# Kernel optimization log

Hardware: AMD Instinct MI355X
Metric: run time of the kernel (lower is better)

## Reference

```python
import jax, jax.numpy as jnp
import numpy as np

B, T, D = 8, 1024, 1024

def setup_inputs() -> dict:
    key = jax.random.key(0)
    ks = jax.random.split(key, 9)
    s = D ** -0.5
    return {
        "x": jax.random.normal(ks[0], (B, T, D), dtype=jnp.float32),
        "w_q": jax.random.normal(ks[1], (D, D), dtype=jnp.float32) * s,
        "b_q": jax.random.normal(ks[2], (D,), dtype=jnp.float32) * 0.02,
        "w_k": jax.random.normal(ks[3], (D, D), dtype=jnp.float32) * s,
        "b_k": jax.random.normal(ks[4], (D,), dtype=jnp.float32) * 0.02,
        "w_v": jax.random.normal(ks[5], (D, D), dtype=jnp.float32) * s,
        "b_v": jax.random.normal(ks[6], (D,), dtype=jnp.float32) * 0.02,
        "w_o": jax.random.normal(ks[7], (D, D), dtype=jnp.float32) * s,
        "b_o": jax.random.normal(ks[8], (D,), dtype=jnp.float32) * 0.02,
    }

def reference(x, w_q, b_q, w_k, b_k, w_v, b_v, w_o, b_o):
    d = x.shape[-1]
    scale = jnp.asarray(d, x.dtype) ** -0.5
    q = jnp.einsum('btd,ed->bte', x, w_q) + b_q  # nn.Linear: x @ W^T + b
    k = jnp.einsum('btd,ed->bte', x, w_k) + b_k
    v = jnp.einsum('btd,ed->bte', x, w_v) + b_v
    t = x.shape[1]
    causal = jnp.tril(jnp.ones((t, t), dtype=bool))  # (T, T)
    scores = jnp.einsum('bqd,bkd->bqk', q, k) * scale
    scores = jnp.where(causal, scores, -jnp.inf)
    attn = jax.nn.softmax(scores, axis=-1)  # max-subtraction folded in
    out = jnp.einsum('bqk,bkd->bqd', attn, v)
    return jnp.einsum('btd,ed->bte', out, w_o) + b_o
```

## Files before the change

kernel.cpp:

```cpp
#include <hip/hip_runtime.h>

typedef unsigned short u16;
typedef __attribute__((ext_vector_type(8))) short short8;
typedef __attribute__((ext_vector_type(4))) float f32x4;


__device__ __forceinline__ u16 f2bf(float f) {
  unsigned u = __builtin_bit_cast(unsigned, f);
  u += 0x7fffu + ((u >> 16) & 1u);
  return (u16)(u >> 16);
}

__device__ __forceinline__ void gload16(const void* g, void* l) {
  __builtin_amdgcn_global_load_lds(
      (const __attribute__((address_space(1))) unsigned*)g,
      (__attribute__((address_space(3))) unsigned*)l, 16, 0, 0);
}


#define PTILE(RB_C, RB_N, DOSTAGE, VM, LAST)                                  \
  {                                                                           \
    char* cA = sA0 + cur * 49152;                                             \
                                                       \
    if (DOSTAGE) {                                                            \
      const int ns = (cur + 2 >= 3) ? cur - 1 : cur + 2;                      \
      char* dA = sA0 + ns * 49152;                                            \
      _Pragma("unroll") for (int j = 0; j < 3; ++j) {                         \
        gload16(ga[j], dA + la[j]); ga[j] += 64; }                            \
    }                                                                         \
    _Pragma("unroll") for (int kk = 0; kk < 2; ++kk)                          \
      _Pragma("unroll") for (int i = 0; i < 2; ++i) {                         \
        const int rm = wr + 32 + i * 16 + l16;                                \
        a1f[kk][i] = *(const short8*)(cA + rm * 128 +                         \
            (((kk << 2) + quad) ^ (rm & 7)) * 16);                            \
      }                                                                       \
    asm volatile("s_waitcnt lgkmcnt(4)" ::: "memory");                        \
    __builtin_amdgcn_sched_barrier(0);                                        \
    __builtin_amdgcn_s_setprio(1);                                            \
    _Pragma("unroll") for (int kk = 0; kk < 2; ++kk)                          \
      _Pragma("unroll") for (int i = 0; i < 2; ++i)                           \
        _Pragma("unroll") for (int j = 0; j < 4; ++j)                         \
          acc[i][j] = __builtin_amdgcn_mfma_f32_16x16x32_bf16(                \
              a0f[kk][i], RB_C[kk][j], acc[i][j], 0, 0, 0);                   \
    __builtin_amdgcn_s_setprio(0);                                            \
                                                       \
    if (DOSTAGE) {                                                            \
      const int ns = (cur + 2 >= 3) ? cur - 1 : cur + 2;                      \
      char* dA = sA0 + ns * 49152; char* dB = dA + 32768;                     \
      gload16(ga[3], dA + la[3]); ga[3] += 64;                                \
      _Pragma("unroll") for (int j = 0; j < 2; ++j) {                         \
        gload16(gb[j], dB + lb[j]); gb[j] += 64; }                            \
    }                                                                         \
    if (!(LAST)) {                                                            \
      asm volatile("s_waitcnt vmcnt(" #VM ") lgkmcnt(0)" ::: "memory");       \
      __builtin_amdgcn_s_barrier();                                           \
      asm volatile("" ::: "memory");                                          \
      const int nc = (cur + 1 >= 3) ? 0 : cur + 1;                            \
      char* nA = sA0 + nc * 49152; char* nB = nA + 32768;                     \
      _Pragma("unroll") for (int kk = 0; kk < 2; ++kk)                        \
        _Pragma("unroll") for (int j = 0; j < 4; ++j) {                       \
          const int rn = wc + j * 16 + l16;                                   \
          RB_N[kk][j] = *(const short8*)(nB + rn * 128 +                      \
              (((kk << 2) + quad) ^ (rn & 7)) * 16);                          \
        }                                                                     \
      _Pragma("unroll") for (int kk = 0; kk < 2; ++kk)                        \
        _Pragma("unroll") for (int i = 0; i < 2; ++i) {                       \
          const int rm = wr + i * 16 + l16;                                   \
          a0f[kk][i] = *(const short8*)(nA + rm * 128 +                       \
              (((kk << 2) + quad) ^ (rm & 7)) * 16);                          \
        }                                                                     \
    } else {                                                                  \
      asm volatile("s_waitcnt lgkmcnt(0)" ::: "memory");                      \
    }                                                                         \
    __builtin_amdgcn_sched_barrier(0);                                        \
    __builtin_amdgcn_s_setprio(1);                                            \
    _Pragma("unroll") for (int kk = 0; kk < 2; ++kk)                          \
      _Pragma("unroll") for (int i = 0; i < 2; ++i)                           \
        _Pragma("unroll") for (int j = 0; j < 4; ++j)                         \
          acc[2 + i][j] = __builtin_amdgcn_mfma_f32_16x16x32_bf16(            \
              a1f[kk][i], RB_C[kk][j], acc[2 + i][j], 0, 0, 0);               \
    __builtin_amdgcn_s_setprio(0);                                            \
    cur = (cur + 1 >= 3) ? 0 : cur + 1;                                       \
  }

__device__ __forceinline__ void gemm_256x128(
    const u16* __restrict__ A, const u16* __restrict__ B,
    int m0, int n0, int ntiles, char* smem, f32x4 acc[4][4])
{
  const int tid  = threadIdx.x;
  const int lane = tid & 63;
  const int quad = lane >> 4;
  const int l16  = lane & 15;
  const int wave = tid >> 6;
  const int wr   = (wave >> 1) << 6;
  const int wc   = (wave & 1) << 6;

  const u16* ga[4]; int la[4];
  const u16* gb[2]; int lb[2];
#pragma unroll
  for (int j = 0; j < 4; ++j) {
    const int L = j * 512 + tid;
    const int r = L >> 3;
    const int c = (L & 7) ^ (r & 7);
    la[j] = L * 16;
    ga[j] = A + (size_t)(m0 + r) * 1024 + c * 8;
  }
#pragma unroll
  for (int j = 0; j < 2; ++j) {
    const int L = j * 512 + tid;
    const int r = L >> 3;
    const int c = (L & 7) ^ (r & 7);
    lb[j] = L * 16;
    gb[j] = B + (size_t)(n0 + r) * 1024 + c * 8;
  }
  char* const sA0 = smem;

  short8 bfr0[2][4], bfr1[2][4];
  short8 a0f[2][2], a1f[2][2];

  {
    char* dA = sA0; char* dB = sA0 + 32768;
#pragma unroll
    for (int j = 0; j < 4; ++j) { gload16(ga[j], dA + la[j]); ga[j] += 64; }
#pragma unroll
    for (int j = 0; j < 2; ++j) { gload16(gb[j], dB + lb[j]); gb[j] += 64; }
    dA = sA0 + 49152; dB = dA + 32768;
#pragma unroll
    for (int j = 0; j < 4; ++j) { gload16(ga[j], dA + la[j]); ga[j] += 64; }
#pragma unroll
    for (int j = 0; j < 2; ++j) { gload16(gb[j], dB + lb[j]); gb[j] += 64; }
  }
  asm volatile("s_waitcnt vmcnt(6)" ::: "memory");
  __builtin_amdgcn_s_barrier();
  asm volatile("" ::: "memory");
  {
    char* nA = sA0; char* nB = sA0 + 32768;
#pragma unroll
    for (int kk = 0; kk < 2; ++kk)
#pragma unroll
      for (int j = 0; j < 4; ++j) {
        const int rn = wc + j * 16 + l16;
        bfr0[kk][j] = *(const short8*)(nB + rn * 128 + (((kk << 2) + quad) ^ (rn & 7)) * 16);
      }
#pragma unroll
    for (int kk = 0; kk < 2; ++kk)
#pragma unroll
      for (int i = 0; i < 2; ++i) {
        const int rm = wr + i * 16 + l16;
        a0f[kk][i] = *(const short8*)(nA + rm * 128 + (((kk << 2) + quad) ^ (rm & 7)) * 16);
      }
  }

  int cur = 0;
  const int npair = (ntiles >> 1) - 1;
#pragma unroll 1
  for (int it = 0; it < npair; ++it) {
    PTILE(bfr0, bfr1, true, 6, false);
    PTILE(bfr1, bfr0, true, 6, false);
  }
  PTILE(bfr0, bfr1, false, 0, false);
  PTILE(bfr1, bfr0, false, 0, true);
  __syncthreads();
}

#define ACC_ZERO4(acc) { _Pragma("unroll") for (int i=0;i<4;++i) \
  _Pragma("unroll") for (int j=0;j<4;++j) \
  _Pragma("unroll") for (int r=0;r<4;++r) acc[i][j][r]=0.f; }

__device__ __forceinline__ void store256x128_bf16(
    f32x4 acc[4][4], const float* bias, int n0,
    u16* C, int m0, char* smem)
{
  const int tid = threadIdx.x, lane = tid & 63, wave = tid >> 6;
  const int quad = lane >> 4, l16 = lane & 15;
  const int wr = (wave >> 1) << 6, wc = (wave & 1) << 6;
  u16* t = (u16*)smem;
#pragma unroll
  for (int j = 0; j < 4; ++j) {
    const int nn = wc + j * 16 + l16;
    const float bj = bias[n0 + nn];
#pragma unroll
    for (int i = 0; i < 4; ++i) {
      const int mm = wr + i * 16 + quad * 4;
#pragma unroll
      for (int r = 0; r < 4; ++r)
        t[(mm + r) * 136 + nn] = f2bf(acc[i][j][r] + bj);
    }
  }
  __syncthreads();
#pragma unroll
  for (int it = 0; it < 8; ++it) {
    const int L = it * 512 + tid;
    const int mm = L >> 4, cc = L & 15;
    *(uint4*)(C + (size_t)(m0 + mm) * 1024 + n0 + cc * 8) =
        *(const uint4*)(t + mm * 136 + cc * 8);
  }
}

__global__ __launch_bounds__(256) void cast_inputs(
    const float* __restrict__ x,  const float* __restrict__ wq,
    const float* __restrict__ wk, const float* __restrict__ wv,
    const float* __restrict__ wo,
    u16* xb, u16* wqb, u16* wkb, u16* wvb, u16* wob, float* rsum)
{
  int b = blockIdx.x;
  if (b < 8) {
    float4 z = {0.f, 0.f, 0.f, 0.f};
    *(float4*)(rsum + (b * 256 + threadIdx.x) * 4) = z;
  }
  const float* src; u16* dst; int base;
  if (b < 4096) { src = x; dst = xb; base = b * 2048; }
  else {
    int r = (b - 4096) >> 9, bb = (b - 4096) & 511;
    base = bb * 2048;
    src = (r == 0) ? wq : (r == 1) ? wk : (r == 2) ? wv : wo;
    dst = (r == 0) ? wqb : (r == 1) ? wkb : (r == 2) ? wvb : wob;
  }
  int i0 = base + threadIdx.x * 8;
  float4 f0 = *(const float4*)(src + i0);
  float4 f1 = *(const float4*)(src + i0 + 4);
  short8 o;
  o[0]=(short)f2bf(f0.x); o[1]=(short)f2bf(f0.y); o[2]=(short)f2bf(f0.z); o[3]=(short)f2bf(f0.w);
  o[4]=(short)f2bf(f1.x); o[5]=(short)f2bf(f1.y); o[6]=(short)f2bf(f1.z); o[7]=(short)f2bf(f1.w);
  *(short8*)(dst + i0) = o;
}

__global__ __launch_bounds__(512, 2) void proj_qkv(
    const u16* __restrict__ xb,
    const u16* __restrict__ wqb, const u16* __restrict__ wkb, const u16* __restrict__ wvb,
    const float* __restrict__ bq, const float* __restrict__ bk, const float* __restrict__ bv,
    u16* q, u16* k, u16* vt)
{
  __shared__ char smem[147456];
  const int z = blockIdx.y;
  const u16* W = (z == 0) ? wqb : (z == 1) ? wkb : wvb;
  const float* bias = (z == 0) ? bq : (z == 1) ? bk : bv;
  const int id = blockIdx.x;
  const int m0 = ((id & 7) * 4 + ((id >> 3) & 3)) * 256;
  const int n0 = (id >> 5) * 128;

  f32x4 acc[4][4]; ACC_ZERO4(acc);
  gemm_256x128(xb, W, m0, n0, 16, smem, acc);

  if (z < 2) {
    store256x128_bf16(acc, bias, n0, (z == 0) ? q : k, m0, smem);
  } else {
    const int tid = threadIdx.x, lane = tid & 63, wave = tid >> 6;
    const int quad = lane >> 4, l16 = lane & 15;
    const int wr = (wave >> 1) << 6, wc = (wave & 1) << 6;
    u16* t = (u16*)smem;
#pragma unroll
    for (int j = 0; j < 4; ++j) {
      const int nn = wc + j * 16 + l16;
      const float bj = bias[n0 + nn];
#pragma unroll
      for (int i = 0; i < 4; ++i) {
        const int mm = wr + i * 16 + quad * 4;
#pragma unroll
        for (int r = 0; r < 4; ++r)
          t[nn * 264 + mm + r] = f2bf(acc[i][j][r] + bj);
      }
    }
    __syncthreads();
    const int b = m0 >> 10, t0 = m0 & 1023;
#pragma unroll
    for (int it = 0; it < 8; ++it) {
      const int L = it * 512 + tid;
      const int nn = L >> 5, cc = L & 31;
      *(uint4*)(vt + ((size_t)b << 20) + (size_t)(n0 + nn) * 1024 + t0 + cc * 8) =
          *(const uint4*)(t + nn * 264 + cc * 8);
    }
  }
}

__global__ __launch_bounds__(512, 2) void qk_exp256(
    const u16* __restrict__ q, const u16* __restrict__ k,
    u16* __restrict__ probs, float* __restrict__ rowsum)
{
  __shared__ char smem[147456];
  const int id = blockIdx.x;
  const int b = id / 20;
  const int t = id - b * 20;
  const int qi = (t < 2) ? 0 : (t < 6) ? 1 : (t < 12) ? 2 : 3;
  const int pre = (qi == 0) ? 0 : (qi == 1) ? 2 : (qi == 2) ? 6 : 12;
  const int kt = t - pre;
  const int m0 = qi * 256, n0 = kt * 128;
  const u16* A = q + ((size_t)b << 20);
  const u16* B = k + ((size_t)b << 20);

  f32x4 acc[4][4]; ACC_ZERO4(acc);
  gemm_256x128(A, B, m0, n0, 16, smem, acc);

  const int tid = threadIdx.x, lane = tid & 63, wave = tid >> 6;
  const int quad = lane >> 4, l16 = lane & 15;
  const int wr = (wave >> 1) << 6, wc = (wave & 1) << 6;

  float part[4][4];
#pragma unroll
  for (int i = 0; i < 4; ++i)
#pragma unroll
    for (int r = 0; r < 4; ++r) part[i][r] = 0.f;

  u16* tl = (u16*)smem;
#pragma unroll
  for (int j = 0; j < 4; ++j) {
    const int nn = wc + j * 16 + l16;
#pragma unroll
    for (int i = 0; i < 4; ++i) {
      const int mm = wr + i * 16 + quad * 4;
#pragma unroll
      for (int r = 0; r < 4; ++r) {
        float e = __expf(acc[i][j][r] * 0.03125f);
        if ((n0 + nn) > (m0 + mm + r)) e = 0.f;
        part[i][r] += e;
        tl[(mm + r) * 136 + nn] = f2bf(e);
      }
    }
  }
  float* rs = rowsum + b * 1024 + m0;
#pragma unroll
  for (int i = 0; i < 4; ++i)
#pragma unroll
    for (int r = 0; r < 4; ++r) {
      float v = part[i][r];
      v += __shfl_xor(v, 1); v += __shfl_xor(v, 2);
      v += __shfl_xor(v, 4); v += __shfl_xor(v, 8);
      if (l16 == 0) atomicAdd(rs + wr + i * 16 + quad * 4 + r, v);
    }
  __syncthreads();
  u16* C = probs + ((size_t)b << 20);
#pragma unroll
  for (int it = 0; it < 8; ++it) {
    const int L = it * 512 + tid;
    const int mm = L >> 4, cc = L & 15;
    *(uint4*)(C + (size_t)(m0 + mm) * 1024 + n0 + cc * 8) =
        *(const uint4*)(tl + mm * 136 + cc * 8);
  }
}

__global__ __launch_bounds__(512, 2) void pv256(
    const u16* __restrict__ probs, const u16* __restrict__ vt,
    const float* __restrict__ rowsum, u16* __restrict__ o)
{
  __shared__ char smem[147456];
  const int id = blockIdx.x;
  const int b = id & 7;
  const int u = id >> 3;
  const int qi = 3 - (u & 3);
  const int nb = u >> 2;
  const int m0 = qi * 256, n0 = nb * 128;
  const int nt = (qi + 1) * 4;
  const u16* A = probs + ((size_t)b << 20);
  const u16* B = vt + ((size_t)b << 20);

  f32x4 acc[4][4]; ACC_ZERO4(acc);
  gemm_256x128(A, B, m0, n0, nt, smem, acc);

  const int tid = threadIdx.x, lane = tid & 63, wave = tid >> 6;
  const int quad = lane >> 4, l16 = lane & 15;
  const int wr = (wave >> 1) << 6, wc = (wave & 1) << 6;
  const float* rs = rowsum + b * 1024 + m0;
  u16* tl = (u16*)smem;
#pragma unroll
  for (int i = 0; i < 4; ++i)
#pragma unroll
    for (int r = 0; r < 4; ++r) {
      const int mm = wr + i * 16 + quad * 4 + r;
      const float inv = 1.0f / rs[mm];
#pragma unroll
      for (int j = 0; j < 4; ++j)
        tl[mm * 136 + wc + j * 16 + l16] = f2bf(acc[i][j][r] * inv);
    }
  __syncthreads();
  u16* C = o + ((size_t)b << 20);
#pragma unroll
  for (int it = 0; it < 8; ++it) {
    const int L = it * 512 + tid;
    const int mm = L >> 4, cc = L & 15;
    *(uint4*)(C + (size_t)(m0 + mm) * 1024 + n0 + cc * 8) =
        *(const uint4*)(tl + mm * 136 + cc * 8);
  }
}

__global__ __launch_bounds__(512, 2) void proj_o(
    const u16* __restrict__ ob, const u16* __restrict__ wob,
    const float* __restrict__ bo, float* __restrict__ out)
{
  __shared__ char smem[147456];
  const int id = blockIdx.x;
  const int m0 = ((id & 7) * 4 + ((id >> 3) & 3)) * 256;
  const int n0 = (id >> 5) * 128;
  f32x4 acc[4][4]; ACC_ZERO4(acc);
  gemm_256x128(ob, wob, m0, n0, 16, smem, acc);

  const int tid = threadIdx.x, lane = tid & 63, wave = tid >> 6;
  const int quad = lane >> 4, l16 = lane & 15;
  const int wr = (wave >> 1) << 6, wc = (wave & 1) << 6;
  float* tf = (float*)smem;
#pragma unroll
  for (int j = 0; j < 4; ++j) {
    const int nn = wc + j * 16 + l16;
    const float bj = bo[n0 + nn];
#pragma unroll
    for (int i = 0; i < 4; ++i)
#pragma unroll
      for (int r = 0; r < 4; ++r)
        tf[(wr + i * 16 + quad * 4 + r) * 132 + nn] = acc[i][j][r] + bj;
  }
  __syncthreads();
#pragma unroll
  for (int it = 0; it < 16; ++it) {
    const int L = it * 512 + tid;
    const int mm = L >> 5, cc = L & 31;
    *(float4*)(out + (size_t)(m0 + mm) * 1024 + n0 + cc * 4) =
        *(const float4*)(tf + mm * 132 + cc * 4);
  }
}

extern "C" void kernel_launch(void* const* d_in, const int* in_sizes, int n_in,
                              void* d_out, int out_size, void* d_ws, size_t ws_size,
                              hipStream_t stream) {
  const float* x  = (const float*)d_in[0];
  const float* wq = (const float*)d_in[1];
  const float* bq = (const float*)d_in[2];
  const float* wk = (const float*)d_in[3];
  const float* bk = (const float*)d_in[4];
  const float* wv = (const float*)d_in[5];
  const float* bv = (const float*)d_in[6];
  const float* wo = (const float*)d_in[7];
  const float* bo = (const float*)d_in[8];
  float* out = (float*)d_out;

  char* ws = (char*)d_ws;
  const size_t MB = 1u << 20;
  u16*  xb  = (u16*)(ws);
  u16*  wqb = (u16*)(ws + 16*MB);
  u16*  wkb = (u16*)(ws + 18*MB);
  u16*  wvb = (u16*)(ws + 20*MB);
  u16*  wob = (u16*)(ws + 22*MB);
  u16*  qb  = (u16*)(ws + 24*MB);
  u16*  kb  = (u16*)(ws + 40*MB);
  u16*  vtb = (u16*)(ws + 56*MB);
  u16*  pr  = (u16*)(ws + 72*MB);
  float* rsum = (float*)(ws + 88*MB);

  cast_inputs<<<6144, 256, 0, stream>>>(x, wq, wk, wv, wo, xb, wqb, wkb, wvb, wob, rsum);
  proj_qkv<<<dim3(256, 3), 512, 0, stream>>>(xb, wqb, wkb, wvb, bq, bk, bv, qb, kb, vtb);
  qk_exp256<<<160, 512, 0, stream>>>(qb, kb, pr, rsum);
  pv256<<<256, 512, 0, stream>>>(pr, vtb, rsum, xb );
  proj_o<<<256, 512, 0, stream>>>(xb, wob, bo, out);
}
```

Measured before the change: 211.9 us.

## Enlarge QKV projection GEMM tile to 256x256 with double-buffered LDS pipeline

Adds a new 256x256-tile GEMM routine for the QKV projection. It uses a two-buffer LDS pipeline and each wave computes a 128x64 sub-tile, which halves the grid to 128x3 blocks. The larger tile raises operand reuse and cuts how often the activations are re-read from global memory. In exchange each thread holds twice the accumulator registers, and with 384 blocks the work may fill the device's compute units less evenly. The Q/K and V-transpose epilogues are rewritten for the wider tile.

```diff
diff --git a/kernel.cpp b/kernel.cpp
--- a/kernel.cpp
+++ b/kernel.cpp
@@ -16,6 +16,8 @@
       (const __attribute__((address_space(1))) unsigned*)g,
       (__attribute__((address_space(3))) unsigned*)l, 16, 0, 0);
 }
+
+#define MFMA16(a, b, c) __builtin_amdgcn_mfma_f32_16x16x32_bf16(a, b, c, 0, 0, 0)
 
 
 #define PTILE(RB_C, RB_N, DOSTAGE, VM, LAST)                                  \
@@ -40,8 +42,7 @@
     _Pragma("unroll") for (int kk = 0; kk < 2; ++kk)                          \
       _Pragma("unroll") for (int i = 0; i < 2; ++i)                           \
         _Pragma("unroll") for (int j = 0; j < 4; ++j)                         \
-          acc[i][j] = __builtin_amdgcn_mfma_f32_16x16x32_bf16(                \
-              a0f[kk][i], RB_C[kk][j], acc[i][j], 0, 0, 0);                   \
+          acc[i][j] = MFMA16(a0f[kk][i], RB_C[kk][j], acc[i][j]);             \
     __builtin_amdgcn_s_setprio(0);                                            \
                                                        \
     if (DOSTAGE) {                                                            \
@@ -77,8 +78,7 @@
     _Pragma("unroll") for (int kk = 0; kk < 2; ++kk)                          \
       _Pragma("unroll") for (int i = 0; i < 2; ++i)                           \
         _Pragma("unroll") for (int j = 0; j < 4; ++j)                         \
-          acc[2 + i][j] = __builtin_amdgcn_mfma_f32_16x16x32_bf16(            \
-              a1f[kk][i], RB_C[kk][j], acc[2 + i][j], 0, 0, 0);               \
+          acc[2 + i][j] = MFMA16(a1f[kk][i], RB_C[kk][j], acc[2 + i][j]);     \
     __builtin_amdgcn_s_setprio(0);                                            \
     cur = (cur + 1 >= 3) ? 0 : cur + 1;                                       \
   }
@@ -163,7 +163,156 @@
   __syncthreads();
 }
 
+
+#define T256(CB, NB, BC, BN, DOSTAGE, LAST)                                   \
+  {                                                                           \
+         \
+    if (DOSTAGE) {                                                            \
+      _Pragma("unroll") for (int j = 0; j < 4; ++j)                           \
+        gload16(gA + j * 65536, (NB) + j * 8192 + t16);                       \
+    }                                                                         \
+    _Pragma("unroll") for (int kk = 0; kk < 2; ++kk)                          \
+      _Pragma("unroll") for (int i = 0; i < 2; ++i) {                         \
+        const int rm = wr + (2 + i) * 16 + l16;                               \
+        aod[kk][i] = *(const short8*)((CB) + rm * 128 +                       \
+            (((kk << 2) + quad) ^ (rm & 7)) * 16);                            \
+      }                                                                       \
+    asm volatile("s_waitcnt lgkmcnt(4)" ::: "memory");                        \
+    __builtin_amdgcn_sched_barrier(0);                                        \
+    __builtin_amdgcn_s_setprio(1);                                            \
+    _Pragma("unroll") for (int kk = 0; kk < 2; ++kk)                          \
+      _Pragma("unroll") for (int i = 0; i < 2; ++i)                           \
+        _Pragma("unroll") for (int j = 0; j < 4; ++j)                         \
+          acc[i][j] = MFMA16(aev[kk][i], BC[kk][j], acc[i][j]);               \
+    __builtin_amdgcn_s_setprio(0);                                            \
+         \
+    if (DOSTAGE) {                                                            \
+      _Pragma("unroll") for (int j = 0; j < 4; ++j)                           \
+        gload16(gB + j * 65536, (NB) + 32768 + j * 8192 + t16);               \
+      gA += 64; gB += 64;                                                     \
+    }                                                                         \
+    _Pragma("unroll") for (int kk = 0; kk < 2; ++kk)                          \
+      _Pragma("unroll") for (int i = 0; i < 2; ++i) {                         \
+        const int rm = wr + (4 + i) * 16 + l16;                               \
+        aev[kk][i] = *(const short8*)((CB) + rm * 128 +                       \
+            (((kk << 2) + quad) ^ (rm & 7)) * 16);                            \
+      }                                                                       \
+    asm volatile("s_waitcnt lgkmcnt(4)" ::: "memory");                        \
+    __builtin_amdgcn_sched_barrier(0);                                        \
+    __builtin_amdgcn_s_setprio(1);                                            \
+    _Pragma("unroll") for (int kk = 0; kk < 2; ++kk)                          \
+      _Pragma("unroll") for (int i = 0; i < 2; ++i)                           \
+        _Pragma("unroll") for (int j = 0; j < 4; ++j)                         \
+          acc[2 + i][j] = MFMA16(aod[kk][i], BC[kk][j], acc[2 + i][j]);       \
+    __builtin_amdgcn_s_setprio(0);                                            \
+                              \
+    _Pragma("unroll") for (int kk = 0; kk < 2; ++kk)                          \
+      _Pragma("unroll") for (int i = 0; i < 2; ++i) {                         \
+        const int rm = wr + (6 + i) * 16 + l16;                               \
+        aod[kk][i] = *(const short8*)((CB) + rm * 128 +                       \
+            (((kk << 2) + quad) ^ (rm & 7)) * 16);                            \
+      }                                                                       \
+    asm volatile("s_waitcnt lgkmcnt(4)" ::: "memory");                        \
+    __builtin_amdgcn_sched_barrier(0);                                        \
+    __builtin_amdgcn_s_setprio(1);                                            \
+    _Pragma("unroll") for (int kk = 0; kk < 2; ++kk)                          \
+      _Pragma("unroll") for (int i = 0; i < 2; ++i)                           \
+        _Pragma("unroll") for (int j = 0; j < 4; ++j)                         \
+          acc[4 + i][j] = MFMA16(aev[kk][i], BC[kk][j], acc[4 + i][j]);       \
+    __builtin_amdgcn_s_setprio(0);                                            \
+     \
+    asm volatile("s_waitcnt vmcnt(0) lgkmcnt(0)" ::: "memory");               \
+    __builtin_amdgcn_sched_barrier(0);                                        \
+    if (!(LAST)) {                                                            \
+      __builtin_amdgcn_s_barrier();                                           \
+      asm volatile("" ::: "memory");                                          \
+      _Pragma("unroll") for (int kk = 0; kk < 2; ++kk)                        \
+        _Pragma("unroll") for (int j = 0; j < 4; ++j) {                       \
+          const int rn = wc + j * 16 + l16;                                   \
+          BN[kk][j] = *(const short8*)((NB) + 32768 + rn * 128 +              \
+              (((kk << 2) + quad) ^ (rn & 7)) * 16);                          \
+        }                                                                     \
+      _Pragma("unroll") for (int kk = 0; kk < 2; ++kk)                        \
+        _Pragma("unroll") for (int i = 0; i < 2; ++i) {                       \
+          const int rm = wr + i * 16 + l16;                                   \
+          aev[kk][i] = *(const short8*)((NB) + rm * 128 +                     \
+              (((kk << 2) + quad) ^ (rm & 7)) * 16);                          \
+        }                                                                     \
+    }                                                                         \
+    __builtin_amdgcn_sched_barrier(0);                                        \
+    __builtin_amdgcn_s_setprio(1);                                            \
+    _Pragma("unroll") for (int kk = 0; kk < 2; ++kk)                          \
+      _Pragma("unroll") for (int i = 0; i < 2; ++i)                           \
+        _Pragma("unroll") for (int j = 0; j < 4; ++j)                         \
+          acc[6 + i][j] = MFMA16(aod[kk][i], BC[kk][j], acc[6 + i][j]);       \
+    __builtin_amdgcn_s_setprio(0);                                            \
+  }
+
+__device__ __forceinline__ void gemm_256x256(
+    const u16* __restrict__ A, const u16* __restrict__ B,
+    int m0, int n0, char* smem, f32x4 acc[8][4])
+{
+  const int tid  = threadIdx.x;
+  const int lane = tid & 63;
+  const int quad = lane >> 4;
+  const int l16  = lane & 15;
+  const int wave = tid >> 6;
+  const int wr   = (wave >> 2) << 7;
+  const int wc   = (wave & 3) << 6;
+
+  const int r0 = tid >> 3;
+  const int c0 = (tid & 7) ^ (r0 & 7);
+  const int t16 = tid * 16;
+  const u16* gA = A + (size_t)(m0 + r0) * 1024 + c0 * 8;
+  const u16* gB = B + (size_t)(n0 + r0) * 1024 + c0 * 8;
+  char* const buf0 = smem;
+  char* const buf1 = smem + 65536;
+
+  short8 bfe[2][4], bfo[2][4];
+  short8 aev[2][2], aod[2][2];
+
+#pragma unroll
+  for (int j = 0; j < 4; ++j) gload16(gA + j * 65536, buf0 + j * 8192 + t16);
+#pragma unroll
+  for (int j = 0; j < 4; ++j) gload16(gB + j * 65536, buf0 + 32768 + j * 8192 + t16);
+  gA += 64; gB += 64;
+#pragma unroll
+  for (int j = 0; j < 4; ++j) gload16(gA + j * 65536, buf1 + j * 8192 + t16);
+#pragma unroll
+  for (int j = 0; j < 4; ++j) gload16(gB + j * 65536, buf1 + 32768 + j * 8192 + t16);
+  gA += 64; gB += 64;
+  asm volatile("s_waitcnt vmcnt(8)" ::: "memory");
+  __builtin_amdgcn_s_barrier();
+  asm volatile("" ::: "memory");
+#pragma unroll
+  for (int kk = 0; kk < 2; ++kk)
+#pragma unroll
+    for (int j = 0; j < 4; ++j) {
+      const int rn = wc + j * 16 + l16;
+      bfe[kk][j] = *(const short8*)(buf0 + 32768 + rn * 128 + (((kk << 2) + quad) ^ (rn & 7)) * 16);
+    }
+#pragma unroll
+  for (int kk = 0; kk < 2; ++kk)
+#pragma unroll
+    for (int i = 0; i < 2; ++i) {
+      const int rm = wr + i * 16 + l16;
+      aev[kk][i] = *(const short8*)(buf0 + rm * 128 + (((kk << 2) + quad) ^ (rm & 7)) * 16);
+    }
+
+  T256(buf0, buf1, bfe, bfo, false, false);
+#pragma unroll 1
+  for (int it = 0; it < 7; ++it) {
+    T256(buf1, buf0, bfo, bfe, true, false);
+    T256(buf0, buf1, bfe, bfo, true, false);
+  }
+  T256(buf1, buf0, bfo, bfe, false, true);
+  __syncthreads();
+}
+
 #define ACC_ZERO4(acc) { _Pragma("unroll") for (int i=0;i<4;++i) \
+  _Pragma("unroll") for (int j=0;j<4;++j) \
+  _Pragma("unroll") for (int r=0;r<4;++r) acc[i][j][r]=0.f; }
+#define ACC_ZERO8(acc) { _Pragma("unroll") for (int i=0;i<8;++i) \
   _Pragma("unroll") for (int j=0;j<4;++j) \
   _Pragma("unroll") for (int r=0;r<4;++r) acc[i][j][r]=0.f; }
 
@@ -231,30 +380,50 @@
     const float* __restrict__ bq, const float* __restrict__ bk, const float* __restrict__ bv,
     u16* q, u16* k, u16* vt)
 {
-  __shared__ char smem[147456];
+  __shared__ char smem[135168];
   const int z = blockIdx.y;
   const u16* W = (z == 0) ? wqb : (z == 1) ? wkb : wvb;
   const float* bias = (z == 0) ? bq : (z == 1) ? bk : bv;
   const int id = blockIdx.x;
   const int m0 = ((id & 7) * 4 + ((id >> 3) & 3)) * 256;
-  const int n0 = (id >> 5) * 128;
-
-  f32x4 acc[4][4]; ACC_ZERO4(acc);
-  gemm_256x128(xb, W, m0, n0, 16, smem, acc);
-
+  const int n0 = (id >> 5) * 256;
+
+  f32x4 acc[8][4]; ACC_ZERO8(acc);
+  gemm_256x256(xb, W, m0, n0, smem, acc);
+
+  const int tid = threadIdx.x, lane = tid & 63, wave = tid >> 6;
+  const int quad = lane >> 4, l16 = lane & 15;
+  const int wr = (wave >> 2) << 7, wc = (wave & 3) << 6;
+  u16* t = (u16*)smem;
   if (z < 2) {
-    store256x128_bf16(acc, bias, n0, (z == 0) ? q : k, m0, smem);
-  } else {
-    const int tid = threadIdx.x, lane = tid & 63, wave = tid >> 6;
-    const int quad = lane >> 4, l16 = lane & 15;
-    const int wr = (wave >> 1) << 6, wc = (wave & 1) << 6;
-    u16* t = (u16*)smem;
+    u16* C = (z == 0) ? q : k;
 #pragma unroll
     for (int j = 0; j < 4; ++j) {
       const int nn = wc + j * 16 + l16;
       const float bj = bias[n0 + nn];
 #pragma unroll
-      for (int i = 0; i < 4; ++i) {
+      for (int i = 0; i < 8; ++i) {
+        const int mm = wr + i * 16 + quad * 4;
+#pragma unroll
+        for (int r = 0; r < 4; ++r)
+          t[(mm + r) * 264 + nn] = f2bf(acc[i][j][r] + bj);
+      }
+    }
+    __syncthreads();
+#pragma unroll
+    for (int it = 0; it < 16; ++it) {
+      const int L = it * 512 + tid;
+      const int mm = L >> 5, cc = L & 31;
+      *(uint4*)(C + (size_t)(m0 + mm) * 1024 + n0 + cc * 8) =
+          *(const uint4*)(t + mm * 264 + cc * 8);
+    }
+  } else {
+#pragma unroll
+    for (int j = 0; j < 4; ++j) {
+      const int nn = wc + j * 16 + l16;
+      const float bj = bias[n0 + nn];
+#pragma unroll
+      for (int i = 0; i < 8; ++i) {
         const int mm = wr + i * 16 + quad * 4;
 #pragma unroll
         for (int r = 0; r < 4; ++r)
@@ -264,7 +433,7 @@
     __syncthreads();
     const int b = m0 >> 10, t0 = m0 & 1023;
 #pragma unroll
-    for (int it = 0; it < 8; ++it) {
+    for (int it = 0; it < 16; ++it) {
       const int L = it * 512 + tid;
       const int nn = L >> 5, cc = L & 31;
       *(uint4*)(vt + ((size_t)b << 20) + (size_t)(n0 + nn) * 1024 + t0 + cc * 8) =
@@ -445,7 +614,7 @@
   float* rsum = (float*)(ws + 88*MB);
 
   cast_inputs<<<6144, 256, 0, stream>>>(x, wq, wk, wv, wo, xb, wqb, wkb, wvb, wob, rsum);
-  proj_qkv<<<dim3(256, 3), 512, 0, stream>>>(xb, wqb, wkb, wvb, bq, bk, bv, qb, kb, vtb);
+  proj_qkv<<<dim3(128, 3), 512, 0, stream>>>(xb, wqb, wkb, wvb, bq, bk, bv, qb, kb, vtb);
   qk_exp256<<<160, 512, 0, stream>>>(qb, kb, pr, rsum);
   pv256<<<256, 512, 0, stream>>>(pr, vtb, rsum, xb );
   proj_o<<<256, 512, 0, stream>>>(xb, wob, bo, out);
```

New measurement: 227.3 us. +7.3%, slower.

## Restructure GEMM main loop into four barrier-synchronized LDS-read/MFMA phases per tile

Applied to the files above, without the earlier changes.

Replaces the double-register-buffered PTILE macro with a TILE4 macro. Each k-tile is split into four phases, each with its own LDS fragment reads, staged global loads, s_barrier pairs and an MFMA cluster. Fragment registers drop from two full sets to one (bfr[2][4], af0/af1), which lowers register pressure. The cost is several extra workgroup barriers per tile and the loss of prefetching the next tile's fragments during the current MFMAs, so LDS latency may be exposed more often.

```diff
diff --git a/kernel.cpp b/kernel.cpp
--- a/kernel.cpp
+++ b/kernel.cpp
@@ -17,69 +17,99 @@
       (__attribute__((address_space(3))) unsigned*)l, 16, 0, 0);
 }
 
-
-#define PTILE(RB_C, RB_N, DOSTAGE, VM, LAST)                                  \
+#define MFMA16(a, b, c) __builtin_amdgcn_mfma_f32_16x16x32_bf16(a, b, c, 0, 0, 0)
+
+
+#define TILE4(DOSTAGE, VM)                                                    \
   {                                                                           \
     char* cA = sA0 + cur * 49152;                                             \
-                                                       \
+    char* cB = cA + 32768;                                                    \
+    char* sD = sA0 + ((cur + 2 >= 3) ? (cur - 1) : (cur + 2)) * 49152;        \
+       \
+    _Pragma("unroll") for (int j = 0; j < 4; ++j) {                           \
+      const int rn = wc + j * 16 + l16;                                       \
+      bfr[0][j] = *(const short8*)(cB + rn * 128 + ((quad ^ (rn & 7)) * 16)); \
+    }                                                                         \
+    _Pragma("unroll") for (int i = 0; i < 2; ++i) {                           \
+      const int rm = wr + i * 16 + l16;                                       \
+      af0[i] = *(const short8*)(cA + rm * 128 + ((quad ^ (rm & 7)) * 16));    \
+    }                                                                         \
     if (DOSTAGE) {                                                            \
-      const int ns = (cur + 2 >= 3) ? cur - 1 : cur + 2;                      \
-      char* dA = sA0 + ns * 49152;                                            \
-      _Pragma("unroll") for (int j = 0; j < 3; ++j) {                         \
-        gload16(ga[j], dA + la[j]); ga[j] += 64; }                            \
-    }                                                                         \
-    _Pragma("unroll") for (int kk = 0; kk < 2; ++kk)                          \
-      _Pragma("unroll") for (int i = 0; i < 2; ++i) {                         \
-        const int rm = wr + 32 + i * 16 + l16;                                \
-        a1f[kk][i] = *(const short8*)(cA + rm * 128 +                         \
-            (((kk << 2) + quad) ^ (rm & 7)) * 16);                            \
-      }                                                                       \
-    asm volatile("s_waitcnt lgkmcnt(4)" ::: "memory");                        \
+      gload16(ga[0], sD + la[0]); ga[0] += 64;                                \
+      gload16(ga[1], sD + la[1]); ga[1] += 64;                                \
+    }                                                                         \
+    asm volatile("s_waitcnt vmcnt(" VM ")" ::: "memory");                     \
+    __builtin_amdgcn_s_barrier();                                             \
+    asm volatile("s_waitcnt lgkmcnt(0)" ::: "memory");                        \
     __builtin_amdgcn_sched_barrier(0);                                        \
     __builtin_amdgcn_s_setprio(1);                                            \
-    _Pragma("unroll") for (int kk = 0; kk < 2; ++kk)                          \
-      _Pragma("unroll") for (int i = 0; i < 2; ++i)                           \
-        _Pragma("unroll") for (int j = 0; j < 4; ++j)                         \
-          acc[i][j] = __builtin_amdgcn_mfma_f32_16x16x32_bf16(                \
-              a0f[kk][i], RB_C[kk][j], acc[i][j], 0, 0, 0);                   \
+    _Pragma("unroll") for (int i = 0; i < 2; ++i)                             \
+      _Pragma("unroll") for (int j = 0; j < 4; ++j)                           \
+        acc[i][j] = MFMA16(af0[i], bfr[0][j], acc[i][j]);                     \
     __builtin_amdgcn_s_setprio(0);                                            \
-                                                       \
+    asm volatile("" ::: "memory");                                            \
+    __builtin_amdgcn_s_barrier();                                             \
+    asm volatile("" ::: "memory");                                            \
+       \
+    _Pragma("unroll") for (int j = 0; j < 4; ++j) {                           \
+      const int rn = wc + j * 16 + l16;                                       \
+      bfr[1][j] = *(const short8*)(cB + rn * 128 + (((4 + quad) ^ (rn & 7)) * 16)); \
+    }                                                                         \
+    _Pragma("unroll") for (int i = 0; i < 2; ++i) {                           \
+      const int rm = wr + i * 16 + l16;                                       \
+      af1[i] = *(const short8*)(cA + rm * 128 + (((4 + quad) ^ (rm & 7)) * 16)); \
+    }                                                                         \
     if (DOSTAGE) {                                                            \
-      const int ns = (cur + 2 >= 3) ? cur - 1 : cur + 2;                      \
-      char* dA = sA0 + ns * 49152; char* dB = dA + 32768;                     \
-      gload16(ga[3], dA + la[3]); ga[3] += 64;                                \
-      _Pragma("unroll") for (int j = 0; j < 2; ++j) {                         \
-        gload16(gb[j], dB + lb[j]); gb[j] += 64; }                            \
-    }                                                                         \
-    if (!(LAST)) {                                                            \
-      asm volatile("s_waitcnt vmcnt(" #VM ") lgkmcnt(0)" ::: "memory");       \
-      __builtin_amdgcn_s_barrier();                                           \
-      asm volatile("" ::: "memory");                                          \
-      const int nc = (cur + 1 >= 3) ? 0 : cur + 1;                            \
-      char* nA = sA0 + nc * 49152; char* nB = nA + 32768;                     \
-      _Pragma("unroll") for (int kk = 0; kk < 2; ++kk)                        \
-        _Pragma("unroll") for (int j = 0; j < 4; ++j) {                       \
-          const int rn = wc + j * 16 + l16;                                   \
-          RB_N[kk][j] = *(const short8*)(nB + rn * 128 +                      \
-              (((kk << 2) + quad) ^ (rn & 7)) * 16);                          \
-        }                                                                     \
-      _Pragma("unroll") for (int kk = 0; kk < 2; ++kk)                        \
-        _Pragma("unroll") for (int i = 0; i < 2; ++i) {                       \
-          const int rm = wr + i * 16 + l16;                                   \
-          a0f[kk][i] = *(const short8*)(nA + rm * 128 +                       \
-              (((kk << 2) + quad) ^ (rm & 7)) * 16);                          \
-        }                                                                     \
-    } else {                                                                  \
-      asm volatile("s_waitcnt lgkmcnt(0)" ::: "memory");                      \
-    }                                                                         \
+      gload16(ga[2], sD + la[2]); ga[2] += 64;                                \
+      gload16(ga[3], sD + la[3]); ga[3] += 64;                                \
+    }                                                                         \
+    __builtin_amdgcn_s_barrier();                                             \
+    asm volatile("s_waitcnt lgkmcnt(0)" ::: "memory");                        \
     __builtin_amdgcn_sched_barrier(0);                                        \
     __builtin_amdgcn_s_setprio(1);                                            \
-    _Pragma("unroll") for (int kk = 0; kk < 2; ++kk)                          \
-      _Pragma("unroll") for (int i = 0; i < 2; ++i)                           \
-        _Pragma("unroll") for (int j = 0; j < 4; ++j)                         \
-          acc[2 + i][j] = __builtin_amdgcn_mfma_f32_16x16x32_bf16(            \
-              a1f[kk][i], RB_C[kk][j], acc[2 + i][j], 0, 0, 0);               \
+    _Pragma("unroll") for (int i = 0; i < 2; ++i)                             \
+      _Pragma("unroll") for (int j = 0; j < 4; ++j)                           \
+        acc[i][j] = MFMA16(af1[i], bfr[1][j], acc[i][j]);                     \
     __builtin_amdgcn_s_setprio(0);                                            \
+    asm volatile("" ::: "memory");                                            \
+    __builtin_amdgcn_s_barrier();                                             \
+    asm volatile("" ::: "memory");                                            \
+       \
+    _Pragma("unroll") for (int i = 0; i < 2; ++i) {                           \
+      const int rm = wr + 32 + i * 16 + l16;                                  \
+      af0[i] = *(const short8*)(cA + rm * 128 + ((quad ^ (rm & 7)) * 16));    \
+    }                                                                         \
+    if (DOSTAGE) {                                                            \
+      gload16(gb[0], sD + 32768 + lb[0]); gb[0] += 64;                        \
+      gload16(gb[1], sD + 32768 + lb[1]); gb[1] += 64;                        \
+    }                                                                         \
+    __builtin_amdgcn_s_barrier();                                             \
+    asm volatile("s_waitcnt lgkmcnt(0)" ::: "memory");                        \
+    __builtin_amdgcn_sched_barrier(0);                                        \
+    __builtin_amdgcn_s_setprio(1);                                            \
+    _Pragma("unroll") for (int i = 0; i < 2; ++i)                             \
+      _Pragma("unroll") for (int j = 0; j < 4; ++j)                           \
+        acc[2 + i][j] = MFMA16(af0[i], bfr[0][j], acc[2 + i][j]);             \
+    __builtin_amdgcn_s_setprio(0);                                            \
+    asm volatile("" ::: "memory");                                            \
+    __builtin_amdgcn_s_barrier();                                             \
+    asm volatile("" ::: "memory");                                            \
+                                \
+    _Pragma("unroll") for (int i = 0; i < 2; ++i) {                           \
+      const int rm = wr + 32 + i * 16 + l16;                                  \
+      af1[i] = *(const short8*)(cA + rm * 128 + (((4 + quad) ^ (rm & 7)) * 16)); \
+    }                                                                         \
+    __builtin_amdgcn_s_barrier();                                             \
+    asm volatile("s_waitcnt lgkmcnt(0)" ::: "memory");                        \
+    __builtin_amdgcn_sched_barrier(0);                                        \
+    __builtin_amdgcn_s_setprio(1);                                            \
+    _Pragma("unroll") for (int i = 0; i < 2; ++i)                             \
+      _Pragma("unroll") for (int j = 0; j < 4; ++j)                           \
+        acc[2 + i][j] = MFMA16(af1[i], bfr[1][j], acc[2 + i][j]);             \
+    __builtin_amdgcn_s_setprio(0);                                            \
+    asm volatile("" ::: "memory");                                            \
+    __builtin_amdgcn_s_barrier();                                             \
+    asm volatile("" ::: "memory");                                            \
     cur = (cur + 1 >= 3) ? 0 : cur + 1;                                       \
   }
 
@@ -115,8 +145,8 @@
   }
   char* const sA0 = smem;
 
-  short8 bfr0[2][4], bfr1[2][4];
-  short8 a0f[2][2], a1f[2][2];
+  short8 bfr[2][4];
+  short8 af0[2], af1[2];
 
   {
     char* dA = sA0; char* dB = sA0 + 32768;
@@ -133,33 +163,14 @@
   asm volatile("s_waitcnt vmcnt(6)" ::: "memory");
   __builtin_amdgcn_s_barrier();
   asm volatile("" ::: "memory");
-  {
-    char* nA = sA0; char* nB = sA0 + 32768;
-#pragma unroll
-    for (int kk = 0; kk < 2; ++kk)
-#pragma unroll
-      for (int j = 0; j < 4; ++j) {
-        const int rn = wc + j * 16 + l16;
-        bfr0[kk][j] = *(const short8*)(nB + rn * 128 + (((kk << 2) + quad) ^ (rn & 7)) * 16);
-      }
-#pragma unroll
-    for (int kk = 0; kk < 2; ++kk)
-#pragma unroll
-      for (int i = 0; i < 2; ++i) {
-        const int rm = wr + i * 16 + l16;
-        a0f[kk][i] = *(const short8*)(nA + rm * 128 + (((kk << 2) + quad) ^ (rm & 7)) * 16);
-      }
-  }
 
   int cur = 0;
-  const int npair = (ntiles >> 1) - 1;
 #pragma unroll 1
-  for (int it = 0; it < npair; ++it) {
-    PTILE(bfr0, bfr1, true, 6, false);
-    PTILE(bfr1, bfr0, true, 6, false);
-  }
-  PTILE(bfr0, bfr1, false, 0, false);
-  PTILE(bfr1, bfr0, false, 0, true);
+  for (int t = 0; t < ntiles - 2; ++t) {
+    TILE4(true, "2");
+  }
+  TILE4(false, "0");
+  TILE4(false, "0");
   __syncthreads();
 }
 
```

Result: slower. 228.9 us (+8.0%).

## Use K-step-32 triple-buffered GEMM for QKV projection with halved LDS

Applied to the files above, without the earlier changes.

Adds a second pipelined GEMM variant for the QKV projection kernel. It stages 32-wide K tiles with a 4-chunk XOR swizzle, which halves the shared-memory footprint, and it raises the launch-bounds occupancy hint from 2 to 4 blocks per CU. The goal is to fit more resident blocks per CU to hide latency. The trade-off is twice as many barrier-separated iterations and half the MFMA work between syncs. The tighter register budget implied by 4 blocks of 512 threads may also cause spills of the 64-float accumulator.

```diff
diff --git a/kernel.cpp b/kernel.cpp
--- a/kernel.cpp
+++ b/kernel.cpp
@@ -16,6 +16,8 @@
       (const __attribute__((address_space(1))) unsigned*)g,
       (__attribute__((address_space(3))) unsigned*)l, 16, 0, 0);
 }
+
+#define MFMA16(a, b, c) __builtin_amdgcn_mfma_f32_16x16x32_bf16(a, b, c, 0, 0, 0)
 
 
 #define PTILE(RB_C, RB_N, DOSTAGE, VM, LAST)                                  \
@@ -40,8 +42,7 @@
     _Pragma("unroll") for (int kk = 0; kk < 2; ++kk)                          \
       _Pragma("unroll") for (int i = 0; i < 2; ++i)                           \
         _Pragma("unroll") for (int j = 0; j < 4; ++j)                         \
-          acc[i][j] = __builtin_amdgcn_mfma_f32_16x16x32_bf16(                \
-              a0f[kk][i], RB_C[kk][j], acc[i][j], 0, 0, 0);                   \
+          acc[i][j] = MFMA16(a0f[kk][i], RB_C[kk][j], acc[i][j]);             \
     __builtin_amdgcn_s_setprio(0);                                            \
                                                        \
     if (DOSTAGE) {                                                            \
@@ -77,8 +78,7 @@
     _Pragma("unroll") for (int kk = 0; kk < 2; ++kk)                          \
       _Pragma("unroll") for (int i = 0; i < 2; ++i)                           \
         _Pragma("unroll") for (int j = 0; j < 4; ++j)                         \
-          acc[2 + i][j] = __builtin_amdgcn_mfma_f32_16x16x32_bf16(            \
-              a1f[kk][i], RB_C[kk][j], acc[2 + i][j], 0, 0, 0);               \
+          acc[2 + i][j] = MFMA16(a1f[kk][i], RB_C[kk][j], acc[2 + i][j]);     \
     __builtin_amdgcn_s_setprio(0);                                            \
     cur = (cur + 1 >= 3) ? 0 : cur + 1;                                       \
   }
@@ -163,6 +163,132 @@
   __syncthreads();
 }
 
+
+#define PTILE32(RB_C, RB_N, DOSTAGE, VM, LAST)                                \
+  {                                                                           \
+    char* cA = sA0 + cur * 24576;                                             \
+      \
+    if (DOSTAGE) {                                                            \
+      char* dA = sA0 + ((cur + 2 >= 3) ? (cur - 1) : (cur + 2)) * 24576;      \
+      gload16(ga[0], dA + la[0]); ga[0] += 32;                                \
+      gload16(ga[1], dA + la[1]); ga[1] += 32;                                \
+    }                                                                         \
+    _Pragma("unroll") for (int i = 0; i < 2; ++i) {                           \
+      const int rm = wr + 32 + i * 16 + l16;                                  \
+      a1f[i] = *(const short8*)(cA + rm * 64 +                                \
+          ((quad ^ ((rm >> 1) & 3)) * 16));                                   \
+    }                                                                         \
+    asm volatile("s_waitcnt lgkmcnt(2)" ::: "memory");                        \
+    __builtin_amdgcn_sched_barrier(0);                                        \
+    __builtin_amdgcn_s_setprio(1);                                            \
+    _Pragma("unroll") for (int i = 0; i < 2; ++i)                             \
+      _Pragma("unroll") for (int j = 0; j < 4; ++j)                           \
+        acc[i][j] = MFMA16(a0f[i], RB_C[j], acc[i][j]);                       \
+    __builtin_amdgcn_s_setprio(0);                                            \
+         \
+    if (DOSTAGE) {                                                            \
+      char* dB = sA0 + ((cur + 2 >= 3) ? (cur - 1) : (cur + 2)) * 24576 + 16384; \
+      gload16(gb0, dB + lb0); gb0 += 32;                                      \
+    }                                                                         \
+    if (!(LAST)) {                                                            \
+      asm volatile("s_waitcnt vmcnt(" #VM ") lgkmcnt(0)" ::: "memory");       \
+      __builtin_amdgcn_s_barrier();                                           \
+      asm volatile("" ::: "memory");                                          \
+      const int nc = (cur + 1 >= 3) ? 0 : cur + 1;                            \
+      char* nA = sA0 + nc * 24576; char* nB = nA + 16384;                     \
+      _Pragma("unroll") for (int j = 0; j < 4; ++j) {                         \
+        const int rn = wc + j * 16 + l16;                                     \
+        RB_N[j] = *(const short8*)(nB + rn * 64 +                             \
+            ((quad ^ ((rn >> 1) & 3)) * 16));                                 \
+      }                                                                       \
+      _Pragma("unroll") for (int i = 0; i < 2; ++i) {                         \
+        const int rm = wr + i * 16 + l16;                                     \
+        a0f[i] = *(const short8*)(nA + rm * 64 +                              \
+            ((quad ^ ((rm >> 1) & 3)) * 16));                                 \
+      }                                                                       \
+    } else {                                                                  \
+      asm volatile("s_waitcnt lgkmcnt(0)" ::: "memory");                      \
+    }                                                                         \
+    __builtin_amdgcn_sched_barrier(0);                                        \
+    __builtin_amdgcn_s_setprio(1);                                            \
+    _Pragma("unroll") for (int i = 0; i < 2; ++i)                             \
+      _Pragma("unroll") for (int j = 0; j < 4; ++j)                           \
+        acc[2 + i][j] = MFMA16(a1f[i], RB_C[j], acc[2 + i][j]);               \
+    __builtin_amdgcn_s_setprio(0);                                            \
+    cur = (cur + 1 >= 3) ? 0 : cur + 1;                                       \
+  }
+
+__device__ __forceinline__ void gemm_256x128_b32(
+    const u16* __restrict__ A, const u16* __restrict__ B,
+    int m0, int n0, char* smem, f32x4 acc[4][4])
+{
+  const int tid  = threadIdx.x;
+  const int lane = tid & 63;
+  const int quad = lane >> 4;
+  const int l16  = lane & 15;
+  const int wave = tid >> 6;
+  const int wr   = (wave >> 1) << 6;
+  const int wc   = (wave & 1) << 6;
+
+  const u16* ga[2]; int la[2];
+  const u16* gb0;   int lb0;
+#pragma unroll
+  for (int j = 0; j < 2; ++j) {
+    const int L = j * 512 + tid;
+    const int r = L >> 2;
+    const int c = (L & 3) ^ ((r >> 1) & 3);
+    la[j] = L * 16;
+    ga[j] = A + (size_t)(m0 + r) * 1024 + c * 8;
+  }
+  {
+    const int r = tid >> 2;
+    const int c = (tid & 3) ^ ((r >> 1) & 3);
+    lb0 = tid * 16;
+    gb0 = B + (size_t)(n0 + r) * 1024 + c * 8;
+  }
+  char* const sA0 = smem;
+
+  short8 bfr0[4], bfr1[4];
+  short8 a0f[2], a1f[2];
+
+  {
+    char* dA = sA0; char* dB = sA0 + 16384;
+#pragma unroll
+    for (int j = 0; j < 2; ++j) { gload16(ga[j], dA + la[j]); ga[j] += 32; }
+    gload16(gb0, dB + lb0); gb0 += 32;
+    dA = sA0 + 24576; dB = dA + 16384;
+#pragma unroll
+    for (int j = 0; j < 2; ++j) { gload16(ga[j], dA + la[j]); ga[j] += 32; }
+    gload16(gb0, dB + lb0); gb0 += 32;
+  }
+  asm volatile("s_waitcnt vmcnt(3)" ::: "memory");
+  __builtin_amdgcn_s_barrier();
+  asm volatile("" ::: "memory");
+  {
+    char* nA = sA0; char* nB = sA0 + 16384;
+#pragma unroll
+    for (int j = 0; j < 4; ++j) {
+      const int rn = wc + j * 16 + l16;
+      bfr0[j] = *(const short8*)(nB + rn * 64 + ((quad ^ ((rn >> 1) & 3)) * 16));
+    }
+#pragma unroll
+    for (int i = 0; i < 2; ++i) {
+      const int rm = wr + i * 16 + l16;
+      a0f[i] = *(const short8*)(nA + rm * 64 + ((quad ^ ((rm >> 1) & 3)) * 16));
+    }
+  }
+
+  int cur = 0;
+#pragma unroll 1
+  for (int it = 0; it < 15; ++it) {
+    PTILE32(bfr0, bfr1, true, 3, false);
+    PTILE32(bfr1, bfr0, true, 3, false);
+  }
+  PTILE32(bfr0, bfr1, false, 0, false);
+  PTILE32(bfr1, bfr0, false, 0, true);
+  __syncthreads();
+}
+
 #define ACC_ZERO4(acc) { _Pragma("unroll") for (int i=0;i<4;++i) \
   _Pragma("unroll") for (int j=0;j<4;++j) \
   _Pragma("unroll") for (int r=0;r<4;++r) acc[i][j][r]=0.f; }
@@ -225,13 +351,13 @@
   *(short8*)(dst + i0) = o;
 }
 
-__global__ __launch_bounds__(512, 2) void proj_qkv(
+__global__ __launch_bounds__(512, 4) void proj_qkv(
     const u16* __restrict__ xb,
     const u16* __restrict__ wqb, const u16* __restrict__ wkb, const u16* __restrict__ wvb,
     const float* __restrict__ bq, const float* __restrict__ bk, const float* __restrict__ bv,
     u16* q, u16* k, u16* vt)
 {
-  __shared__ char smem[147456];
+  __shared__ char smem[73728];
   const int z = blockIdx.y;
   const u16* W = (z == 0) ? wqb : (z == 1) ? wkb : wvb;
   const float* bias = (z == 0) ? bq : (z == 1) ? bk : bv;
@@ -240,7 +366,7 @@
   const int n0 = (id >> 5) * 128;
 
   f32x4 acc[4][4]; ACC_ZERO4(acc);
-  gemm_256x128(xb, W, m0, n0, 16, smem, acc);
+  gemm_256x128_b32(xb, W, m0, n0, smem, acc);
 
   if (z < 2) {
     store256x128_bf16(acc, bias, n0, (z == 0) ? q : k, m0, smem);
```

Result: slower. 226.1 us (+6.7%).
